# Kernel tuning notes

Measured on AMD Instinct MI355X. Metric: run time of the kernel, lower is better.

Reference implementation:

```python
import jax, jax.numpy as jnp
import numpy as np

N = 100000   # num_nodes (also in_channels of layer 1, since x=None)
R = 50       # num_relations
B = 30       # num_bases
H = 16       # hidden channels
C = 8        # num_classes
E = 1600000  # num_edges (avg degree 16)


def setup_inputs() -> dict:
    key = jax.random.key(0)
    ks = jax.random.split(key, 10)
    s = 0.05
    edge_index = jax.random.randint(ks[0], (2, E), 0, N, dtype=jnp.int32)
    edge_type = jax.random.randint(ks[1], (E,), 0, R, dtype=jnp.int32)
    # layer 1 (in=N because x is None -> node-index / embedding mode)
    basis1 = jax.random.normal(ks[2], (B, N, H), jnp.float32) * s
    comp1 = jax.random.normal(ks[3], (R, B), jnp.float32) * s
    root1 = jax.random.normal(ks[4], (N, H), jnp.float32) * s
    bias1 = jnp.zeros((H,), jnp.float32)
    # layer 2 (in=H, out=C)
    basis2 = jax.random.normal(ks[5], (B, H, C), jnp.float32) * s
    comp2 = jax.random.normal(ks[6], (R, B), jnp.float32) * s
    root2 = jax.random.normal(ks[7], (H, C), jnp.float32) * s
    bias2 = jnp.zeros((C,), jnp.float32)
    return dict(edge_index=edge_index, edge_type=edge_type,
                basis1=basis1, comp1=comp1, root1=root1, bias1=bias1,
                basis2=basis2, comp2=comp2, root2=root2, bias2=bias2)


def reference(edge_index, edge_type, basis1, comp1, root1, bias1,
              basis2, comp2, root2, bias2):
    src, dst = edge_index[0], edge_index[1]
    # PyG RGCNConv uses aggr='mean' per relation: each message is divided by
    # the number of same-relation incoming edges at its target node.
    seg = dst * R + edge_type                                   # [E] (node, rel) segment id
    cnt = jax.ops.segment_sum(jnp.ones((E,), jnp.float32), seg, num_segments=N * R)
    inv = 1.0 / jnp.maximum(cnt, 1.0)                           # [N*R]
    inv_e = inv[seg][:, None]                                   # [E,1]

    # ---- layer 1: x = None -> message_e = weight[rel_e][src_e] ----
    w1 = jnp.einsum('rb,bnh->rnh', comp1, basis1)               # [R,N,H] basis-combined weights
    msg1 = w1[edge_type, src] * inv_e                           # [E,H]
    h = jax.ops.segment_sum(msg1, dst, num_segments=N)          # [N,H]
    h = h + root1 + bias1                                       # root embedding + bias
    # NOTE: source does `x.relu()` without assignment -> no-op; faithfully omitted.

    # ---- layer 2: mean-aggregate per (node, relation), then per-relation matmul ----
    w2 = jnp.einsum('rb,bhc->rhc', comp2, basis2)               # [R,H,C]
    agg = jax.ops.segment_sum(h[src] * inv_e, seg, num_segments=N * R)
    agg = agg.reshape(N, R, H)                                  # [N,R,H]
    out = jnp.einsum('nrh,rhc->nc', agg, w2) + h @ root2 + bias2
    return out
```

## Files before the change

kernel.cpp:

```cpp
#include <hip/hip_runtime.h>

#define NREL   50
#define NBASE  30
#define HID    16
#define NCLS   8

#define SHIFT   9
#define BWID    (1 << SHIFT)
#define NBUKMAX 512
#define TILE    4096
#define EPB     16
#define W2T     56
#define C1P     36

typedef float vf4 __attribute__((ext_vector_type(4)));


__global__ void compute_w2_kernel(const float* __restrict__ comp2,
                                  const float* __restrict__ basis2,
                                  float* __restrict__ w2) {
    int i = blockIdx.x * blockDim.x + threadIdx.x;
    if (i >= NREL * HID * NCLS) return;
    int r  = i / (HID * NCLS);
    int hc = i % (HID * NCLS);
    float acc = 0.f;
    #pragma unroll
    for (int b = 0; b < NBASE; ++b)
        acc += comp2[r * NBASE + b] * basis2[b * HID * NCLS + hc];
    w2[i] = acc;
}


__global__ void ghist_kernel(const int* __restrict__ src,
                             const int* __restrict__ dst,
                             int* __restrict__ hs, int* __restrict__ hd,
                             int E, int nbuk) {
    __shared__ int lhs[NBUKMAX], lhd[NBUKMAX];
    for (int j = threadIdx.x; j < nbuk; j += blockDim.x) { lhs[j] = 0; lhd[j] = 0; }
    __syncthreads();
    for (long e = (long)blockIdx.x * blockDim.x + threadIdx.x; e < E;
         e += (long)gridDim.x * blockDim.x) {
        atomicAdd(&lhs[src[e] >> SHIFT], 1);
        atomicAdd(&lhd[dst[e] >> SHIFT], 1);
    }
    __syncthreads();
    for (int j = threadIdx.x; j < nbuk; j += blockDim.x) {
        if (lhs[j]) atomicAdd(&hs[j], lhs[j]);
        if (lhd[j]) atomicAdd(&hd[j], lhd[j]);
    }
}

__global__ void scanbuk_kernel(const int* __restrict__ hs, const int* __restrict__ hd,
                               int* __restrict__ gcs, int* __restrict__ bases_s,
                               int* __restrict__ based, int* __restrict__ gcd,
                               int nbuk, int E) {
    __shared__ int a[NBUKMAX], b[NBUKMAX];
    int tid = threadIdx.x;
    for (int j = tid; j < nbuk; j += blockDim.x) { a[j] = hs[j]; b[j] = hd[j]; }
    __syncthreads();
    if (tid == 0) {
        int run = 0;
        for (int i = 0; i < nbuk; ++i) { int v = a[i]; a[i] = run; run += v; }
        run = 0;
        for (int i = 0; i < nbuk; ++i) { int v = b[i]; b[i] = run; run += v; }
    }
    __syncthreads();
    for (int j = tid; j < nbuk; j += blockDim.x) {
        gcs[j] = a[j]; bases_s[j] = a[j];
        based[j] = b[j]; gcd[j] = b[j];
    }
    if (tid == 0) { bases_s[nbuk] = E; based[nbuk] = E; }
}

__global__ void pass1_kernel(const int* __restrict__ src,
                             const int* __restrict__ dst,
                             const int* __restrict__ et,
                             int* __restrict__ gcur,
                             int* __restrict__ Ax0, int* __restrict__ Ad0, int E) {
    __shared__ int lhist[NBUKMAX], lbase[NBUKMAX], lcur[NBUKMAX];
    int tid = threadIdx.x;
    for (int j = tid; j < NBUKMAX; j += 256) { lhist[j] = 0; lcur[j] = 0; }
    __syncthreads();
    int px[EPB], pd[EPB]; int bk[EPB];
    long e0 = (long)blockIdx.x * TILE;
    #pragma unroll
    for (int j = 0; j < EPB; ++j) {
        long e = e0 + j * 256 + tid;
        if (e < E) {
            int s = src[e], d = dst[e], t = et[e];
            px[j] = s | (t << 17);
            pd[j] = d;
            bk[j] = s >> SHIFT;
            atomicAdd(&lhist[bk[j]], 1);
        } else bk[j] = -1;
    }
    __syncthreads();
    for (int j = tid; j < NBUKMAX; j += 256)
        if (lhist[j] > 0) lbase[j] = atomicAdd(&gcur[j], lhist[j]);
    __syncthreads();
    #pragma unroll
    for (int j = 0; j < EPB; ++j) {
        if (bk[j] >= 0) {
            int r = atomicAdd(&lcur[bk[j]], 1);
            int pos = lbase[bk[j]] + r;
            Ax0[pos] = px[j];
            Ad0[pos] = pd[j];
        }
    }
}

__global__ void pass1b_kernel(const int* __restrict__ Ax0,
                              const int* __restrict__ Ad0,
                              const int* __restrict__ bases_s,
                              int* __restrict__ Ax, int* __restrict__ Ad,
                              int* __restrict__ rowptr_s, int N, int E) {
    __shared__ int lh[BWID], sA[BWID], sB[BWID];
    int blk = blockIdx.x, tid = threadIdx.x;
    int k0 = bases_s[blk], k1 = bases_s[blk + 1], cnt = k1 - k0;
    for (int j = tid; j < BWID; j += 256) lh[j] = 0;
    __syncthreads();
    for (int i = tid; i < cnt; i += 256) {
        int slow = Ax0[k0 + i] & (BWID - 1);
        atomicAdd(&lh[slow], 1);
    }
    __syncthreads();
    for (int j = tid; j < BWID; j += 256) sA[j] = lh[j];
    __syncthreads();
    int* cur = sA; int* oth = sB;
    for (int off = 1; off < BWID; off <<= 1) {
        for (int j = tid; j < BWID; j += 256)
            oth[j] = cur[j] + (j >= off ? cur[j - off] : 0);
        __syncthreads();
        int* t_ = cur; cur = oth; oth = t_;
    }
    for (int j = tid; j < BWID; j += 256) {
        int excl = cur[j] - lh[j];
        oth[j] = excl;
        int s = blk * BWID + j;
        if (s < N) rowptr_s[s] = k0 + excl;
    }
    __syncthreads();
    for (int i = tid; i < cnt; i += 256) {
        int x = Ax0[k0 + i], d = Ad0[k0 + i];
        int slow = x & (BWID - 1);
        int pos = atomicAdd(&oth[slow], 1);
        Ax[k0 + pos] = x;
        Ad[k0 + pos] = d;
    }
    if (blk == 0 && tid == 0) rowptr_s[N] = E;
}

__global__ void pass2_kernel(const int* __restrict__ Ax,
                             const int* __restrict__ Ad,
                             int* __restrict__ gcur, int2* __restrict__ B, int E) {
    __shared__ int lhist[NBUKMAX], lbase[NBUKMAX], lcur[NBUKMAX];
    int tid = threadIdx.x;
    for (int j = tid; j < NBUKMAX; j += 256) { lhist[j] = 0; lcur[j] = 0; }
    __syncthreads();
    int2 p[EPB]; int bk[EPB];
    long e0 = (long)blockIdx.x * TILE;
    #pragma unroll
    for (int j = 0; j < EPB; ++j) {
        long e = e0 + j * 256 + tid;
        if (e < E) {
            int x = Ax[e];
            int d = Ad[e];
            p[j] = make_int2(x, (int)e | ((d & (BWID - 1)) << 21));
            bk[j] = d >> SHIFT;
            atomicAdd(&lhist[bk[j]], 1);
        } else bk[j] = -1;
    }
    __syncthreads();
    for (int j = tid; j < NBUKMAX; j += 256)
        if (lhist[j] > 0) lbase[j] = atomicAdd(&gcur[j], lhist[j]);
    __syncthreads();
    #pragma unroll
    for (int j = 0; j < EPB; ++j) {
        if (bk[j] >= 0) {
            int r = atomicAdd(&lcur[bk[j]], 1);
            B[lbase[bk[j]] + r] = p[j];
        }
    }
}

__global__ void pass3_kernel(const int2* __restrict__ B,
                             const int* __restrict__ based,
                             int2* __restrict__ e2, int* __restrict__ rowptr,
                             int N, int E) {
    __shared__ int lh[BWID], sA[BWID], sB[BWID];
    int blk = blockIdx.x, tid = threadIdx.x;
    int k0 = based[blk], k1 = based[blk + 1], cnt = k1 - k0;
    for (int j = tid; j < BWID; j += 256) lh[j] = 0;
    __syncthreads();
    for (int i = tid; i < cnt; i += 256) {
        int dlow = ((unsigned)B[k0 + i].y) >> 21;
        atomicAdd(&lh[dlow], 1);
    }
    __syncthreads();
    for (int j = tid; j < BWID; j += 256) sA[j] = lh[j];
    __syncthreads();
    int* cur = sA; int* oth = sB;
    for (int off = 1; off < BWID; off <<= 1) {
        for (int j = tid; j < BWID; j += 256)
            oth[j] = cur[j] + (j >= off ? cur[j - off] : 0);
        __syncthreads();
        int* t_ = cur; cur = oth; oth = t_;
    }
    for (int j = tid; j < BWID; j += 256) {
        int excl = cur[j] - lh[j];
        oth[j] = excl;
        int d = blk * BWID + j;
        if (d < N) rowptr[d] = k0 + excl;
    }
    __syncthreads();
    for (int i = tid; i < cnt; i += 256) {
        int2 b = B[k0 + i];
        int dlow = ((unsigned)b.y) >> 21;
        int pos = atomicAdd(&oth[dlow], 1);
        e2[k0 + pos] = make_int2(b.x, b.y & 0x1FFFFF);
    }
    if (blk == 0 && tid == 0) rowptr[N] = E;
}

__global__ void layer1A_node_kernel(const int* __restrict__ Ax,
                                    const int* __restrict__ rowptr_s,
                                    const float* __restrict__ comp1,
                                    const float* __restrict__ basis1,
                                    float* __restrict__ msg, int N) {
    __shared__ float c1s[NREL * C1P];
    for (int i = threadIdx.x; i < NREL * C1P; i += blockDim.x) {
        int t = i / C1P, b = i % C1P;
        c1s[i] = (b < NBASE) ? comp1[t * NBASE + b] : 0.f;
    }
    __syncthreads();
    int gid = threadIdx.x >> 4;
    int l   = threadIdx.x & 15;
    int s = blockIdx.x * 16 + gid;
    if (s >= N) return;
    int k0 = rowptr_s[s], k1 = rowptr_s[s + 1];
    if (k0 == k1) return;

    vf4 b4[8];
    {
        long stride = (long)N * HID;
        const float* bp = basis1 + (long)s * HID + l;
        float breg[32];
        #pragma unroll
        for (int b = 0; b < NBASE; ++b)
            breg[b] = bp[(long)b * stride];
        #pragma unroll
        for (int b = NBASE; b < 32; ++b) breg[b] = 0.f;
        #pragma unroll
        for (int i = 0; i < 8; ++i)
            b4[i] = (vf4){breg[4*i], breg[4*i+1], breg[4*i+2], breg[4*i+3]};
    }

    int k = k0;
    for (; k + 4 <= k1; k += 4) {
        int t0 = ((unsigned)Ax[k + 0]) >> 17;
        int t1 = ((unsigned)Ax[k + 1]) >> 17;
        int t2 = ((unsigned)Ax[k + 2]) >> 17;
        int t3 = ((unsigned)Ax[k + 3]) >> 17;
        const vf4* c0 = reinterpret_cast<const vf4*>(c1s + t0 * C1P);
        const vf4* c1 = reinterpret_cast<const vf4*>(c1s + t1 * C1P);
        const vf4* c2 = reinterpret_cast<const vf4*>(c1s + t2 * C1P);
        const vf4* c3 = reinterpret_cast<const vf4*>(c1s + t3 * C1P);
        vf4 a0 = {0.f,0.f,0.f,0.f}, a1 = a0, a2 = a0, a3 = a0;
        #pragma unroll
        for (int i = 0; i < 8; ++i) {
            a0 += c0[i] * b4[i];
            a1 += c1[i] * b4[i];
            a2 += c2[i] * b4[i];
            a3 += c3[i] * b4[i];
        }
        float r0 = (a0.x + a0.y) + (a0.z + a0.w);
        float r1 = (a1.x + a1.y) + (a1.z + a1.w);
        float r2 = (a2.x + a2.y) + (a2.z + a2.w);
        float r3 = (a3.x + a3.y) + (a3.z + a3.w);
        __builtin_nontemporal_store(r0, &msg[(long)(k + 0) * HID + l]);
        __builtin_nontemporal_store(r1, &msg[(long)(k + 1) * HID + l]);
        __builtin_nontemporal_store(r2, &msg[(long)(k + 2) * HID + l]);
        __builtin_nontemporal_store(r3, &msg[(long)(k + 3) * HID + l]);
    }
    for (; k < k1; ++k) {
        int t = ((unsigned)Ax[k]) >> 17;
        const vf4* cr4 = reinterpret_cast<const vf4*>(c1s + t * C1P);
        vf4 acc4 = {0.f, 0.f, 0.f, 0.f};
        #pragma unroll
        for (int i = 0; i < 8; ++i)
            acc4 += cr4[i] * b4[i];
        float acc = (acc4.x + acc4.y) + (acc4.z + acc4.w);
        __builtin_nontemporal_store(acc, &msg[(long)k * HID + l]);
    }
}

__global__ void layer1B_kernel(const int2* __restrict__ e2,
                               const int* __restrict__ rowptr,
                               const float* __restrict__ msg,
                               const float* __restrict__ root1,
                               const float* __restrict__ bias1,
                               float* __restrict__ h, float* __restrict__ sinv, int N) {
    long gid = (long)blockIdx.x * blockDim.x + threadIdx.x;
    int d = (int)(gid >> 3);
    if (d >= N) return;
    int q = (int)(gid & 7);
    int k0 = rowptr[d], k1 = rowptr[d + 1];

    float acc[HID];
    #pragma unroll
    for (int i = 0; i < HID; ++i) acc[i] = 0.f;

    for (int k = k0 + q; k < k1; k += 8) {
        int2 v = e2[k];
        unsigned t = ((unsigned)v.x) >> 17;
        int c = 0;
        for (int j = k0; j < k1; ++j)
            c += ((((unsigned)e2[j].x) >> 17) == t);
        float inv = 1.0f / (float)c;
        sinv[k] = inv;
        const vf4* m4 = reinterpret_cast<const vf4*>(msg + (long)v.y * HID);
        #pragma unroll
        for (int p = 0; p < HID / 4; ++p) {
            vf4 m = __builtin_nontemporal_load(m4 + p);
            acc[4 * p + 0] += inv * m.x; acc[4 * p + 1] += inv * m.y;
            acc[4 * p + 2] += inv * m.z; acc[4 * p + 3] += inv * m.w;
        }
    }

    #pragma unroll
    for (int i = 0; i < HID; ++i) {
        acc[i] += __shfl_xor(acc[i], 1);
        acc[i] += __shfl_xor(acc[i], 2);
        acc[i] += __shfl_xor(acc[i], 4);
    }

    if (q == 0) {
        float4* h4 = reinterpret_cast<float4*>(h + (size_t)d * HID);
        #pragma unroll
        for (int p = 0; p < HID / 4; ++p) {
            float4 r = *reinterpret_cast<const float4*>(root1 + (size_t)d * HID + p * 4);
            float4 bv = *reinterpret_cast<const float4*>(bias1 + p * 4);
            h4[p] = make_float4(acc[4 * p + 0] + r.x + bv.x,
                                acc[4 * p + 1] + r.y + bv.y,
                                acc[4 * p + 2] + r.z + bv.z,
                                acc[4 * p + 3] + r.w + bv.w);
        }
    }
}

__global__ void layer2_kernel(const int2* __restrict__ e2,
                              const int* __restrict__ rowptr,
                              const float* __restrict__ sinv,
                              const float* __restrict__ w2,
                              const float* __restrict__ h,
                              const float* __restrict__ root2,
                              const float* __restrict__ bias2,
                              float* __restrict__ out, int N) {
    __shared__ float w2s[HID * NCLS * W2T];
    for (int i = threadIdx.x; i < NREL * HID * NCLS; i += blockDim.x) {
        int t = i / (HID * NCLS);
        int hc = i % (HID * NCLS);
        w2s[hc * W2T + t] = w2[i];
    }
    __syncthreads();

    int gid = blockIdx.x * blockDim.x + threadIdx.x;
    int d = gid >> 2;
    if (d >= N) return;
    int q = gid & 3;
    int k0 = rowptr[d], k1 = rowptr[d + 1];

    float acc[NCLS];
    #pragma unroll
    for (int c = 0; c < NCLS; ++c) acc[c] = 0.f;

    for (int k = k0 + q; k < k1; k += 4) {
        int2 v = e2[k];
        int s = v.x & 0x1FFFF;
        int t = ((unsigned)v.x) >> 17;
        float inv = sinv[k];
        const float4* h4 = reinterpret_cast<const float4*>(h + (size_t)s * HID);
        float tmp[NCLS];
        #pragma unroll
        for (int c = 0; c < NCLS; ++c) tmp[c] = 0.f;
        #pragma unroll
        for (int p = 0; p < HID / 4; ++p) {
            float4 hv = h4[p];
            float hvv[4] = {hv.x, hv.y, hv.z, hv.w};
            #pragma unroll
            for (int j = 0; j < 4; ++j) {
                int i = 4 * p + j;
                #pragma unroll
                for (int c = 0; c < NCLS; ++c)
                    tmp[c] += hvv[j] * w2s[(i * NCLS + c) * W2T + t];
            }
        }
        #pragma unroll
        for (int c = 0; c < NCLS; ++c) acc[c] += inv * tmp[c];
    }

    #pragma unroll
    for (int c = 0; c < NCLS; ++c) {
        acc[c] += __shfl_xor(acc[c], 1);
        acc[c] += __shfl_xor(acc[c], 2);
    }

    if (q == 0) {
        const float4* h4 = reinterpret_cast<const float4*>(h + (size_t)d * HID);
        #pragma unroll
        for (int p = 0; p < HID / 4; ++p) {
            float4 hv = h4[p];
            float hvv[4] = {hv.x, hv.y, hv.z, hv.w};
            #pragma unroll
            for (int j = 0; j < 4; ++j) {
                int i = 4 * p + j;
                #pragma unroll
                for (int c = 0; c < NCLS; ++c)
                    acc[c] += hvv[j] * root2[i * NCLS + c];
            }
        }
        #pragma unroll
        for (int c = 0; c < NCLS; ++c) acc[c] += bias2[c];
        float4* o4 = reinterpret_cast<float4*>(out + (size_t)d * NCLS);
        o4[0] = make_float4(acc[0], acc[1], acc[2], acc[3]);
        o4[1] = make_float4(acc[4], acc[5], acc[6], acc[7]);
    }
}


extern "C" void kernel_launch(void* const* d_in, const int* in_sizes, int n_in,
                              void* d_out, int out_size, void* d_ws, size_t ws_size,
                              hipStream_t stream) {
    const int*   edge_index = (const int*)  d_in[0];
    const int*   edge_type  = (const int*)  d_in[1];
    const float* basis1     = (const float*)d_in[2];
    const float* comp1      = (const float*)d_in[3];
    const float* root1      = (const float*)d_in[4];
    const float* bias1      = (const float*)d_in[5];
    const float* basis2     = (const float*)d_in[6];
    const float* comp2      = (const float*)d_in[7];
    const float* root2      = (const float*)d_in[8];
    const float* bias2      = (const float*)d_in[9];
    float* out = (float*)d_out;

    const int E = in_sizes[1];
    const int N = in_sizes[4] / HID;
    const int nbuk = (N + BWID - 1) >> SHIFT;
    const int* src = edge_index;
    const int* dst = edge_index + E;

    char* base = (char*)d_ws;
    size_t off = 0;
    auto alloc = [&](size_t bytes, size_t align) -> char* {
        off = (off + align - 1) & ~(align - 1);
        char* p = base + off;
        off += bytes;
        return p;
    };
    int*  hs       = (int*)  alloc((size_t)NBUKMAX * 4, 4);
    int*  hd       = (int*)  alloc((size_t)NBUKMAX * 4, 4);
    int*  gcs      = (int*)  alloc((size_t)NBUKMAX * 4, 4);
    int*  gcd      = (int*)  alloc((size_t)NBUKMAX * 4, 4);
    int*  bases_s  = (int*)  alloc((size_t)(NBUKMAX + 1) * 4, 4);
    int*  based    = (int*)  alloc((size_t)(NBUKMAX + 1) * 4, 4);
    int*  rowptr   = (int*)  alloc((size_t)(N + 1) * 4, 4);
    int*  rowptr_s = (int*)  alloc((size_t)(N + 1) * 4, 4);
    float* w2      = (float*)alloc((size_t)NREL * HID * NCLS * 4, 16);
    float* h       = (float*)alloc((size_t)N * HID * 4, 16);
    float* sinv    = (float*)alloc((size_t)E * 4, 4);
    int*  Ax0      = (int*)  alloc((size_t)E * 4, 4);
    int*  Ad0      = (int*)  alloc((size_t)E * 4, 4);
    int*  Ax       = (int*)  alloc((size_t)E * 4, 4);
    int*  Ad       = (int*)  alloc((size_t)E * 4, 4);
    int2* B        = (int2*) alloc((size_t)E * 8, 8);
    int2* e2       = (int2*) alloc((size_t)E * 8, 8);
    float* msg     = (float*)alloc((size_t)E * HID * 4, 16);

    hipMemsetAsync(hs, 0, (size_t)NBUKMAX * 2 * 4, stream);

    {   int M = NREL * HID * NCLS;
        compute_w2_kernel<<<(M + 255) / 256, 256, 0, stream>>>(comp2, basis2, w2);
    }
    ghist_kernel<<<2048, 256, 0, stream>>>(src, dst, hs, hd, E, nbuk);
    scanbuk_kernel<<<1, 256, 0, stream>>>(hs, hd, gcs, bases_s, based, gcd, nbuk, E);

    int nblk = (E + TILE - 1) / TILE;
    pass1_kernel<<<nblk, 256, 0, stream>>>(src, dst, edge_type, gcs, Ax0, Ad0, E);
    pass1b_kernel<<<nbuk, 256, 0, stream>>>(Ax0, Ad0, bases_s, Ax, Ad, rowptr_s, N, E);
    pass2_kernel<<<nblk, 256, 0, stream>>>(Ax, Ad, gcd, B, E);
    pass3_kernel<<<nbuk, 256, 0, stream>>>(B, based, e2, rowptr, N, E);

    {   int blocks = (N + 15) / 16;
        layer1A_node_kernel<<<blocks, 256, 0, stream>>>(
            Ax, rowptr_s, comp1, basis1, msg, N);
    }
    {   long total = (long)N * 8;
        layer1B_kernel<<<(int)((total + 255) / 256), 256, 0, stream>>>(
            e2, rowptr, msg, root1, bias1, h, sinv, N);
    }
    {   long total = (long)N * 4;
        layer2_kernel<<<(int)((total + 255) / 256), 256, 0, stream>>>(
            e2, rowptr, sinv, w2, h, root2, bias2, out, N);
    }
}
```

Before: 418.0 us.

## Scatter layer-1 messages directly into destination-sorted order via permutation

pass3 now records, for each source-sorted edge index, its position in the destination-sorted order (perm) and emits a compact 4-byte edge array instead of int2. layer1A writes each message row to its destination-sorted slot, so layer1B reads msg contiguously instead of gathering by source-sorted index. The aim is to turn the random 64-byte gather in layer1B into streaming reads and shrink the edge arrays. In exchange, layer1A's stores become scattered and an extra perm array is written and read.

Result: slower. 433.5 us (+3.7%).

```diff
diff --git a/kernel.cpp b/kernel.cpp
--- a/kernel.cpp
+++ b/kernel.cpp
@@ -185,8 +185,8 @@
 
 __global__ void pass3_kernel(const int2* __restrict__ B,
                              const int* __restrict__ based,
-                             int2* __restrict__ e2, int* __restrict__ rowptr,
-                             int N, int E) {
+                             int* __restrict__ e2x, int* __restrict__ perm,
+                             int* __restrict__ rowptr, int N, int E) {
     __shared__ int lh[BWID], sA[BWID], sB[BWID];
     int blk = blockIdx.x, tid = threadIdx.x;
     int k0 = based[blk], k1 = based[blk + 1], cnt = k1 - k0;
@@ -216,13 +216,15 @@
     for (int i = tid; i < cnt; i += 256) {
         int2 b = B[k0 + i];
         int dlow = ((unsigned)b.y) >> 21;
-        int pos = atomicAdd(&oth[dlow], 1);
-        e2[k0 + pos] = make_int2(b.x, b.y & 0x1FFFFF);
+        int pos = k0 + atomicAdd(&oth[dlow], 1);
+        e2x[pos] = b.x;
+        perm[b.y & 0x1FFFFF] = pos;
     }
     if (blk == 0 && tid == 0) rowptr[N] = E;
 }
 
 __global__ void layer1A_node_kernel(const int* __restrict__ Ax,
+                                    const int* __restrict__ perm,
                                     const int* __restrict__ rowptr_s,
                                     const float* __restrict__ comp1,
                                     const float* __restrict__ basis1,
@@ -261,6 +263,7 @@
         int t1 = ((unsigned)Ax[k + 1]) >> 17;
         int t2 = ((unsigned)Ax[k + 2]) >> 17;
         int t3 = ((unsigned)Ax[k + 3]) >> 17;
+        int p0 = perm[k + 0], p1 = perm[k + 1], p2 = perm[k + 2], p3 = perm[k + 3];
         const vf4* c0 = reinterpret_cast<const vf4*>(c1s + t0 * C1P);
         const vf4* c1 = reinterpret_cast<const vf4*>(c1s + t1 * C1P);
         const vf4* c2 = reinterpret_cast<const vf4*>(c1s + t2 * C1P);
@@ -277,24 +280,25 @@
         float r1 = (a1.x + a1.y) + (a1.z + a1.w);
         float r2 = (a2.x + a2.y) + (a2.z + a2.w);
         float r3 = (a3.x + a3.y) + (a3.z + a3.w);
-        __builtin_nontemporal_store(r0, &msg[(long)(k + 0) * HID + l]);
-        __builtin_nontemporal_store(r1, &msg[(long)(k + 1) * HID + l]);
-        __builtin_nontemporal_store(r2, &msg[(long)(k + 2) * HID + l]);
-        __builtin_nontemporal_store(r3, &msg[(long)(k + 3) * HID + l]);
+        __builtin_nontemporal_store(r0, &msg[(long)p0 * HID + l]);
+        __builtin_nontemporal_store(r1, &msg[(long)p1 * HID + l]);
+        __builtin_nontemporal_store(r2, &msg[(long)p2 * HID + l]);
+        __builtin_nontemporal_store(r3, &msg[(long)p3 * HID + l]);
     }
     for (; k < k1; ++k) {
         int t = ((unsigned)Ax[k]) >> 17;
+        int p = perm[k];
         const vf4* cr4 = reinterpret_cast<const vf4*>(c1s + t * C1P);
         vf4 acc4 = {0.f, 0.f, 0.f, 0.f};
         #pragma unroll
         for (int i = 0; i < 8; ++i)
             acc4 += cr4[i] * b4[i];
         float acc = (acc4.x + acc4.y) + (acc4.z + acc4.w);
-        __builtin_nontemporal_store(acc, &msg[(long)k * HID + l]);
-    }
-}
-
-__global__ void layer1B_kernel(const int2* __restrict__ e2,
+        __builtin_nontemporal_store(acc, &msg[(long)p * HID + l]);
+    }
+}
+
+__global__ void layer1B_kernel(const int* __restrict__ e2x,
                                const int* __restrict__ rowptr,
                                const float* __restrict__ msg,
                                const float* __restrict__ root1,
@@ -311,14 +315,13 @@
     for (int i = 0; i < HID; ++i) acc[i] = 0.f;
 
     for (int k = k0 + q; k < k1; k += 8) {
-        int2 v = e2[k];
-        unsigned t = ((unsigned)v.x) >> 17;
+        unsigned t = ((unsigned)e2x[k]) >> 17;
         int c = 0;
         for (int j = k0; j < k1; ++j)
-            c += ((((unsigned)e2[j].x) >> 17) == t);
+            c += ((((unsigned)e2x[j]) >> 17) == t);
         float inv = 1.0f / (float)c;
         sinv[k] = inv;
-        const vf4* m4 = reinterpret_cast<const vf4*>(msg + (long)v.y * HID);
+        const vf4* m4 = reinterpret_cast<const vf4*>(msg + (long)k * HID);
         #pragma unroll
         for (int p = 0; p < HID / 4; ++p) {
             vf4 m = __builtin_nontemporal_load(m4 + p);
@@ -348,7 +351,7 @@
     }
 }
 
-__global__ void layer2_kernel(const int2* __restrict__ e2,
+__global__ void layer2_kernel(const int* __restrict__ e2x,
                               const int* __restrict__ rowptr,
                               const float* __restrict__ sinv,
                               const float* __restrict__ w2,
@@ -375,9 +378,9 @@
     for (int c = 0; c < NCLS; ++c) acc[c] = 0.f;
 
     for (int k = k0 + q; k < k1; k += 4) {
-        int2 v = e2[k];
-        int s = v.x & 0x1FFFF;
-        int t = ((unsigned)v.x) >> 17;
+        int v = e2x[k];
+        int s = v & 0x1FFFF;
+        int t = ((unsigned)v) >> 17;
         float inv = sinv[k];
         const float4* h4 = reinterpret_cast<const float4*>(h + (size_t)s * HID);
         float tmp[NCLS];
@@ -472,8 +475,9 @@
     int*  Ad0      = (int*)  alloc((size_t)E * 4, 4);
     int*  Ax       = (int*)  alloc((size_t)E * 4, 4);
     int*  Ad       = (int*)  alloc((size_t)E * 4, 4);
+    int*  perm     = (int*)  alloc((size_t)E * 4, 4);
     int2* B        = (int2*) alloc((size_t)E * 8, 8);
-    int2* e2       = (int2*) alloc((size_t)E * 8, 8);
+    int*  e2x      = (int*)  alloc((size_t)E * 4, 4);
     float* msg     = (float*)alloc((size_t)E * HID * 4, 16);
 
     hipMemsetAsync(hs, 0, (size_t)NBUKMAX * 2 * 4, stream);
@@ -488,18 +492,18 @@
     pass1_kernel<<<nblk, 256, 0, stream>>>(src, dst, edge_type, gcs, Ax0, Ad0, E);
     pass1b_kernel<<<nbuk, 256, 0, stream>>>(Ax0, Ad0, bases_s, Ax, Ad, rowptr_s, N, E);
     pass2_kernel<<<nblk, 256, 0, stream>>>(Ax, Ad, gcd, B, E);
-    pass3_kernel<<<nbuk, 256, 0, stream>>>(B, based, e2, rowptr, N, E);
+    pass3_kernel<<<nbuk, 256, 0, stream>>>(B, based, e2x, perm, rowptr, N, E);
 
     {   int blocks = (N + 15) / 16;
         layer1A_node_kernel<<<blocks, 256, 0, stream>>>(
-            Ax, rowptr_s, comp1, basis1, msg, N);
+            Ax, perm, rowptr_s, comp1, basis1, msg, N);
     }
     {   long total = (long)N * 8;
         layer1B_kernel<<<(int)((total + 255) / 256), 256, 0, stream>>>(
-            e2, rowptr, msg, root1, bias1, h, sinv, N);
+            e2x, rowptr, msg, root1, bias1, h, sinv, N);
     }
     {   long total = (long)N * 4;
         layer2_kernel<<<(int)((total + 255) / 256), 256, 0, stream>>>(
-            e2, rowptr, sinv, w2, h, root2, bias2, out, N);
-    }
-}
+            e2x, rowptr, sinv, w2, h, root2, bias2, out, N);
+    }
+}
```
